# Performance work log

Hardware: AMD Instinct MI355X
Metric: run time of the kernel (lower is better)

## Reference

```python
import jax, jax.numpy as jnp
import numpy as np

D_MODEL = 1024
NUM_HEADS = 16
HEAD_DIM = D_MODEL // NUM_HEADS
B, S = 2, 2048


def setup_inputs() -> dict:
    key = jax.random.key(0)
    ks = jax.random.split(key, 8)
    scale = 1.0 / np.sqrt(D_MODEL)
    inp = {
        "query": jax.random.normal(ks[0], (B, S, D_MODEL), jnp.float32),
        "key": jax.random.normal(ks[1], (B, S, D_MODEL), jnp.float32),
        "value": jax.random.normal(ks[2], (B, S, D_MODEL), jnp.float32),
        # causal mask, broadcastable over batch and heads
        "mask": jnp.tril(jnp.ones((S, S), dtype=bool))[None, None, :, :],
        # torch nn.Linear weights: y = x @ W.T (+ b)
        "Wq": jax.random.normal(ks[3], (D_MODEL, D_MODEL), jnp.float32) * scale,
        "Wk": jax.random.normal(ks[4], (D_MODEL, D_MODEL), jnp.float32) * scale,
        "Wv": jax.random.normal(ks[5], (D_MODEL, D_MODEL), jnp.float32) * scale,
        "Wo": jax.random.normal(ks[6], (D_MODEL, D_MODEL), jnp.float32) * scale,
        "bo": jax.random.normal(ks[7], (D_MODEL,), jnp.float32) * scale,
    }
    return inp


def _split_heads(x):
    b, s, _ = x.shape
    return x.reshape(b, s, NUM_HEADS, HEAD_DIM).transpose(0, 2, 1, 3)  # [B,H,S,Dh]


def reference(query, key, value, mask, Wq, Wk, Wv, Wo, bo):
    q = _split_heads(query @ Wq.T)
    k = _split_heads(key @ Wk.T)
    v = _split_heads(value @ Wv.T)
    scores = jnp.einsum("bhqd,bhkd->bhqk", q, k) / jnp.sqrt(jnp.float32(HEAD_DIM))
    scores = jnp.where(mask, scores, jnp.float32(-jnp.inf))
    attn = jax.nn.softmax(scores, axis=-1)
    out = jnp.einsum("bhqk,bhkd->bhqd", attn, v)  # [B,H,S,Dh]
    out = out.transpose(0, 2, 1, 3).reshape(query.shape[0], q.shape[2], D_MODEL)
    return out @ Wo.T + bo
```

## Files before the change

kernel.cpp:

```cpp
#include <hip/hip_runtime.h>
#include <hip/hip_bf16.h>

#define DM   1024
#define NH   16
#define HD   64
#define SEQ  2048
#define BATCH 2
#define MTOT (BATCH*SEQ)

typedef unsigned short u16;
typedef __attribute__((ext_vector_type(8))) short bf16x8;
typedef __attribute__((ext_vector_type(4))) float f32x4;

__device__ __forceinline__ float bf2f(u16 h) {
  union { unsigned int i; float f; } u; u.i = ((unsigned int)h) << 16; return u.f;
}
__device__ __forceinline__ u16 f2bf(float f) {
  union { float f; unsigned int i; } u; u.f = f;
  unsigned int r = u.i + 0x7fffu + ((u.i >> 16) & 1u);
  return (u16)(r >> 16);
}
__device__ __forceinline__ unsigned int pk2(float lo, float hi) {
  union { float f; unsigned int u; } a, b; a.f = lo; b.f = hi;
  return ((a.u + 0x8000u) >> 16) | ((b.u + 0x8000u) & 0xFFFF0000u);
}

__global__ void detect_dtype(const u16* __restrict__ q, int* __restrict__ flag) {
  const int lane = threadIdx.x & 63;
  int cnt = 0;
  for (int i = 0; i < 8; i++) {
    int e = (q[i*64 + lane] >> 7) & 0xFF;
    unsigned long long m = __ballot(e >= 0x6E && e <= 0x8F);
    cnt += __popcll(m);
  }
  if (lane == 0) *flag = (cnt >= 400) ? 1 : 0;
}

__device__ __forceinline__ uint4 load8_bf16(const void* base, size_t elemOff, bool isf32) {
  if (!isf32) return *(const uint4*)((const u16*)base + elemOff);
  const float* f = (const float*)base + elemOff;
  f32x4 a = *(const f32x4*)f;
  f32x4 b = *(const f32x4*)(f + 4);
  union { u16 h[8]; uint4 v; } r;
  r.h[0]=f2bf(a[0]); r.h[1]=f2bf(a[1]); r.h[2]=f2bf(a[2]); r.h[3]=f2bf(a[3]);
  r.h[4]=f2bf(b[0]); r.h[5]=f2bf(b[1]); r.h[6]=f2bf(b[2]); r.h[7]=f2bf(b[3]);
  return r.v;
}

__global__ __launch_bounds__(256) void prep(
    const void* __restrict__ q, const void* __restrict__ k, const void* __restrict__ v,
    const void* __restrict__ wq, const void* __restrict__ wk, const void* __restrict__ wv,
    const void* __restrict__ wo, const void* __restrict__ bo,
    u16* __restrict__ Xq, u16* __restrict__ Xk, u16* __restrict__ Xv,
    u16* __restrict__ Wqb, u16* __restrict__ Wkb, u16* __restrict__ Wvb, u16* __restrict__ Wob,
    float* __restrict__ biasf, const int* __restrict__ dflag)
{
  const bool isf32 = (*dflag == 0);
  const int z = blockIdx.z;
  if (z == 7) {
    if (blockIdx.x == 0) {
      for (int i = threadIdx.x; i < DM; i += 256)
        biasf[i] = isf32 ? ((const float*)bo)[i] : bf2f(((const u16*)bo)[i]);
    }
    return;
  }
  const void* src; u16* dst; size_t n;
  switch (z) {
    case 0: src=q;  dst=Xq;  n=(size_t)MTOT*DM; break;
    case 1: src=k;  dst=Xk;  n=(size_t)MTOT*DM; break;
    case 2: src=v;  dst=Xv;  n=(size_t)MTOT*DM; break;
    case 3: src=wq; dst=Wqb; n=(size_t)DM*DM;   break;
    case 4: src=wk; dst=Wkb; n=(size_t)DM*DM;   break;
    case 5: src=wv; dst=Wvb; n=(size_t)DM*DM;   break;
    default: src=wo; dst=Wob; n=(size_t)DM*DM;  break;
  }
  const size_t stride = (size_t)gridDim.x * 256 * 8;
  for (size_t i = ((size_t)blockIdx.x * 256 + threadIdx.x) * 8; i < n; i += stride)
    *(uint4*)(dst + i) = load8_bf16(src, i, isf32);
}

__device__ __forceinline__ void gld16(const u16* g, u16* l) {
  __builtin_amdgcn_global_load_lds(
      (const __attribute__((address_space(1))) void*)g,
      (__attribute__((address_space(3))) void*)l, 16, 0, 0);
}

template<int MODE>
__global__ __launch_bounds__(256) void gemm128(
    const u16* __restrict__ X0, const u16* __restrict__ X1, const u16* __restrict__ X2,
    const u16* __restrict__ W0, const u16* __restrict__ W1, const u16* __restrict__ W2,
    const float* __restrict__ biasf,
    u16* __restrict__ F0, u16* __restrict__ F1, u16* __restrict__ F2,
    void* __restrict__ outP, const int* __restrict__ dflag)
{
  __shared__ u16 As[128*32];
  __shared__ u16 Bs[128*32];

  const u16* X; const u16* W; u16* outF = nullptr; int zz = 0;
  if (MODE == 0) {
    zz = blockIdx.z;
    X    = (zz==0) ? X0 : ((zz==1) ? X1 : X2);
    W    = (zz==0) ? W0 : ((zz==1) ? W1 : W2);
    outF = (zz==0) ? F0 : ((zz==1) ? F1 : F2);
  } else { X = X0; W = W0; }

  const int tid = threadIdx.x;
  const int wave = tid >> 6, lane = tid & 63, quad = lane >> 4, l16 = lane & 15;
  const int wr = wave >> 1, wc = wave & 1;
  const int m0 = blockIdx.y * 128, n0 = blockIdx.x * 128;

  const int sg = ((lane & 3) ^ ((lane >> 3) & 3)) * 8;
  const int rS = wave*32 + (lane >> 2);
  const u16* gA0 = X + (size_t)(m0 + rS)*DM + sg;
  const u16* gA1 = X + (size_t)(m0 + rS + 16)*DM + sg;
  const u16* gB0 = W + (size_t)(n0 + rS)*DM + sg;
  const u16* gB1 = W + (size_t)(n0 + rS + 16)*DM + sg;
  u16* lA0 = &As[wave*1024];
  u16* lA1 = &As[wave*1024 + 512];
  u16* lB0 = &Bs[wave*1024];
  u16* lB1 = &Bs[wave*1024 + 512];

  const int xslot8 = (quad ^ ((l16 >> 1) & 3)) * 8;

  f32x4 acc[4][4];
#pragma unroll
  for (int i = 0; i < 4; i++)
#pragma unroll
    for (int j = 0; j < 4; j++) { acc[i][j][0]=0.f; acc[i][j][1]=0.f; acc[i][j][2]=0.f; acc[i][j][3]=0.f; }

  for (int k0 = 0; k0 < DM; k0 += 32) {
    __syncthreads();
    gld16(gA0 + k0, lA0);
    gld16(gA1 + k0, lA1);
    gld16(gB0 + k0, lB0);
    gld16(gB1 + k0, lB1);
    __syncthreads();

    bf16x8 af[4], bfr[4];
#pragma unroll
    for (int fr = 0; fr < 4; fr++)
      af[fr] = *(const bf16x8*)&As[(wr*64 + fr*16 + l16)*32 + xslot8];
#pragma unroll
    for (int fc = 0; fc < 4; fc++)
      bfr[fc] = *(const bf16x8*)&Bs[(wc*64 + fc*16 + l16)*32 + xslot8];
#pragma unroll
    for (int fr = 0; fr < 4; fr++)
#pragma unroll
      for (int fc = 0; fc < 4; fc++)
        acc[fr][fc] = __builtin_amdgcn_mfma_f32_16x16x32_bf16(af[fr], bfr[fc], acc[fr][fc], 0, 0, 0);
  }

  const bool isf32 = (MODE == 1) && (*dflag == 0);
#pragma unroll
  for (int fr = 0; fr < 4; fr++) {
#pragma unroll
    for (int rr = 0; rr < 4; rr++) {
      const int m = m0 + wr*64 + fr*16 + quad*4 + rr;
#pragma unroll
      for (int fc = 0; fc < 4; fc++) {
        const int n = n0 + wc*64 + fc*16 + l16;
        float vv = acc[fr][fc][rr];
        if (MODE == 0) {
          const int b = m >> 11, s = m & (SEQ-1), h = n >> 6, d = n & (HD-1);
          if (zz == 2)
            outF[((size_t)(b*NH + h)*HD + d)*SEQ + s] = f2bf(vv);
          else
            outF[((size_t)(b*NH + h)*SEQ + s)*HD + d] = f2bf(vv);
        } else {
          vv += biasf[n];
          if (isf32) ((float*)outP)[(size_t)m*DM + n] = vv;
          else       ((u16*)outP)[(size_t)m*DM + n]   = f2bf(vv);
        }
      }
    }
  }
}

__global__ __launch_bounds__(256) void attn_mfma(
    const u16* __restrict__ Qb, const u16* __restrict__ Kb,
    const u16* __restrict__ Vtb,
    u16* __restrict__ Opart, float* __restrict__ mlpart)
{
  __shared__ u16 Qs[64][72];
  __shared__ u16 Ks[64][72];
  __shared__ u16 Vs[64][72];
  __shared__ u16 Ps[4][16][72];

  const int bh = blockIdx.x;
  const int pr = blockIdx.y, z = blockIdx.z;
  const u16* Qp = Qb  + (size_t)bh * SEQ * HD;
  const u16* Kp = Kb  + (size_t)bh * SEQ * HD;
  const u16* Vp = Vtb + (size_t)bh * HD * SEQ;

  const int tid  = threadIdx.x;
  const int wave = tid >> 6, lane = tid & 63, quad = lane >> 4, l16 = lane & 15;
  const int sr = tid >> 3, sc = (tid & 7) * 8;
  const float SC2 = 0.1803368801f;

  for (int ph = 0; ph < 2; ph++) {
    const int qt = ph ? (31 - pr) : pr;
    const int n = qt + 1, half = (n + 1) >> 1;
    const int klo = z ? half : 0, khi = z ? n : half;
    const int q0 = qt * 64;

    __syncthreads();
    *(uint4*)&Qs[sr][sc]      = *(const uint4*)&Qp[(size_t)(q0 + sr)*HD + sc];
    *(uint4*)&Qs[sr + 32][sc] = *(const uint4*)&Qp[(size_t)(q0 + sr + 32)*HD + sc];

    const int ql = wave*16 + l16;
    const int qg = q0 + ql;
    f32x4 O[4];
#pragma unroll
    for (int u = 0; u < 4; u++) { O[u][0]=0.f; O[u][1]=0.f; O[u][2]=0.f; O[u][3]=0.f; }
    float mi = -__builtin_inff(), li = 0.f;

    for (int kt = klo; kt < khi; kt++) {
      __syncthreads();
      *(uint4*)&Ks[sr][sc]      = *(const uint4*)&Kp[(size_t)(kt*64 + sr)*HD + sc];
      *(uint4*)&Ks[sr + 32][sc] = *(const uint4*)&Kp[(size_t)(kt*64 + sr + 32)*HD + sc];
      *(uint4*)&Vs[sr][sc]      = *(const uint4*)&Vp[(size_t)sr*SEQ + kt*64 + sc];
      *(uint4*)&Vs[sr + 32][sc] = *(const uint4*)&Vp[(size_t)(sr + 32)*SEQ + kt*64 + sc];
      __syncthreads();

      f32x4 st[4];
#pragma unroll
      for (int t = 0; t < 4; t++) { st[t][0]=0.f; st[t][1]=0.f; st[t][2]=0.f; st[t][3]=0.f; }
#pragma unroll
      for (int s = 0; s < 2; s++) {
        bf16x8 bq = *(const bf16x8*)&Qs[ql][s*32 + quad*8];
#pragma unroll
        for (int t = 0; t < 4; t++) {
          bf16x8 ak = *(const bf16x8*)&Ks[t*16 + l16][s*32 + quad*8];
          st[t] = __builtin_amdgcn_mfma_f32_16x16x32_bf16(ak, bq, st[t], 0, 0, 0);
        }
      }

      float v[4][4];
#pragma unroll
      for (int t = 0; t < 4; t++)
#pragma unroll
        for (int r = 0; r < 4; r++) v[t][r] = st[t][r] * SC2;
      if (kt == qt) {
#pragma unroll
        for (int t = 0; t < 4; t++)
#pragma unroll
          for (int r = 0; r < 4; r++)
            if (kt*64 + t*16 + quad*4 + r > qg) v[t][r] = -__builtin_inff();
      }
      float mx = v[0][0];
#pragma unroll
      for (int t = 0; t < 4; t++)
#pragma unroll
        for (int r = 0; r < 4; r++) mx = fmaxf(mx, v[t][r]);
      mx = fmaxf(mx, __shfl_xor(mx, 16));
      mx = fmaxf(mx, __shfl_xor(mx, 32));
      const float nm = fmaxf(mi, mx);
      const float al = exp2f(mi - nm);
      float ps = 0.f;
#pragma unroll
      for (int t = 0; t < 4; t++) {
        float p0 = exp2f(v[t][0] - nm), p1 = exp2f(v[t][1] - nm);
        float p2 = exp2f(v[t][2] - nm), p3 = exp2f(v[t][3] - nm);
        ps += (p0 + p1) + (p2 + p3);
        uint2 u2; u2.x = pk2(p0, p1); u2.y = pk2(p2, p3);
        *(uint2*)&Ps[wave][l16][t*16 + quad*4] = u2;
      }
      ps += __shfl_xor(ps, 16);
      ps += __shfl_xor(ps, 32);
      li = li * al + ps;
      mi = nm;
#pragma unroll
      for (int u = 0; u < 4; u++) {
        O[u][0] *= al; O[u][1] *= al; O[u][2] *= al; O[u][3] *= al;
      }
      __syncthreads();

#pragma unroll
      for (int s = 0; s < 2; s++) {
        bf16x8 bp = *(const bf16x8*)&Ps[wave][l16][s*32 + quad*8];
#pragma unroll
        for (int u = 0; u < 4; u++) {
          bf16x8 av = *(const bf16x8*)&Vs[u*16 + l16][s*32 + quad*8];
          O[u] = __builtin_amdgcn_mfma_f32_16x16x32_bf16(av, bp, O[u], 0, 0, 0);
        }
      }
    }

    const int pi = (bh*32 + qt)*2 + z;
    u16* op = Opart + (size_t)pi*4096 + ql*64;
#pragma unroll
    for (int u = 0; u < 4; u++) {
      uint2 u2; u2.x = pk2(O[u][0], O[u][1]); u2.y = pk2(O[u][2], O[u][3]);
      *(uint2*)&op[u*16 + quad*4] = u2;
    }
    if (quad == 0) {
      float2 ml2; ml2.x = mi; ml2.y = li;
      *(float2*)&mlpart[(size_t)pi*128 + ql*2] = ml2;
    }
  }
}

__global__ __launch_bounds__(64) void attn_merge(
    const u16* __restrict__ Opart, const float* __restrict__ mlpart,
    u16* __restrict__ aO)
{
  const int g = blockIdx.x;
  const int bh = g & 31, qt = g >> 5;
  const int b = bh >> 4, h = bh & 15;
  const int t = threadIdx.x;
  const int pi0 = (bh*32 + qt)*2, pi1 = pi0 + 1;

  const float2 ml0 = *(const float2*)&mlpart[(size_t)pi0*128 + t*2];
  const float2 ml1 = *(const float2*)&mlpart[(size_t)pi1*128 + t*2];
  const float M = fmaxf(ml0.x, ml1.x);
  float w0 = exp2f(ml0.x - M), w1 = exp2f(ml1.x - M);
  const float inv = 1.0f / (w0*ml0.y + w1*ml1.y);
  w0 *= inv; w1 *= inv;

  const u16* o0 = Opart + (size_t)pi0*4096 + t*64;
  const u16* o1 = Opart + (size_t)pi1*4096 + t*64;
  u16* out = aO + (size_t)(b*SEQ + qt*64 + t)*DM + h*HD;
#pragma unroll
  for (int d0 = 0; d0 < 64; d0 += 8) {
    union { uint4 v; u16 h[8]; } a, c; union { uint4 v; u16 h[8]; } bb;
    a.v  = *(const uint4*)&o0[d0];
    bb.v = *(const uint4*)&o1[d0];
#pragma unroll
    for (int j = 0; j < 8; j += 2) {
      float x0 = w0*bf2f(a.h[j])   + w1*bf2f(bb.h[j]);
      float x1 = w0*bf2f(a.h[j+1]) + w1*bf2f(bb.h[j+1]);
      unsigned int pk = pk2(x0, x1);
      c.h[j] = (u16)(pk & 0xFFFF); c.h[j+1] = (u16)(pk >> 16);
    }
    *(uint4*)&out[d0] = c.v;
  }
}

extern "C" void kernel_launch(void* const* d_in, const int* in_sizes, int n_in,
                              void* d_out, int out_size, void* d_ws, size_t ws_size,
                              hipStream_t stream) {
  const void* q  = d_in[0];
  const void* k  = d_in[1];
  const void* v  = d_in[2];
  const void* wq = d_in[4];
  const void* wk = d_in[5];
  const void* wv = d_in[6];
  const void* wo = d_in[7];
  const void* bo = d_in[8];

  const size_t TX = (size_t)MTOT*DM;
  const size_t TW = (size_t)DM*DM;
  u16* ws  = (u16*)d_ws;
  u16* Xq  = ws;
  u16* Xk  = ws + TX;
  u16* Xv  = ws + 2*TX;
  u16* Wqb = ws + 3*TX;
  u16* Wkb = Wqb + TW;
  u16* Wvb = Wqb + 2*TW;
  u16* Wob = Wqb + 3*TW;
  u16* Qw  = ws + 3*TX + 4*TW;
  u16* Kw  = Qw + TX;
  u16* Vt  = Qw + 2*TX;
  u16*   Opart  = Xk;
  float* mlpart = (float*)Wqb;
  u16*   aO     = Xq;
  float* biasf  = (float*)(Qw + 3*TX);
  int*   fl     = (int*)(biasf + DM);

  dim3 blk(256);
  detect_dtype<<<1, 64, 0, stream>>>((const u16*)q, fl);
  prep<<<dim3(512, 1, 8), blk, 0, stream>>>(q, k, v, wq, wk, wv, wo, bo,
      Xq, Xk, Xv, Wqb, Wkb, Wvb, Wob, biasf, fl);
  gemm128<0><<<dim3(DM/128, MTOT/128, 3), blk, 0, stream>>>(
      Xq, Xk, Xv, Wqb, Wkb, Wvb, nullptr, Qw, Kw, Vt, nullptr, fl);
  attn_mfma<<<dim3(BATCH*NH, 16, 2), blk, 0, stream>>>(Qw, Kw, Vt, Opart, mlpart);
  attn_merge<<<dim3(32*32), dim3(64), 0, stream>>>(Opart, mlpart, aO);
  gemm128<1><<<dim3(DM/128, MTOT/128, 1), blk, 0, stream>>>(
      aO, nullptr, nullptr, Wob, nullptr, nullptr, biasf, nullptr, nullptr, nullptr, d_out, fl);
}
```

Measured before the change: 255.0 us.

## Stage attention tiles via direct global-to-LDS loads with XOR swizzle, fold scale into Q

The attention kernel now loads Q, K and V tiles with direct global-to-LDS copies (gld16) into unpadded, XOR-swizzled shared arrays, replacing register-staged copies into padded arrays. The softmax scale is folded into the Q projection epilogue, and the block barrier before the PV MMA becomes a per-wave lgkmcnt wait, since each wave only reads its own P rows. The V-transposed projection output is first staged through a swizzled shared tile so it can be written with coalesced 16-byte stores. This cuts staging instructions, barriers and scattered 2-byte stores, but the swizzle and the wave-local sync have to be exactly right, and scaling before bf16 rounding changes numerics slightly.

```diff
diff --git a/kernel.cpp b/kernel.cpp
--- a/kernel.cpp
+++ b/kernel.cpp
@@ -11,6 +11,8 @@
 typedef unsigned short u16;
 typedef __attribute__((ext_vector_type(8))) short bf16x8;
 typedef __attribute__((ext_vector_type(4))) float f32x4;
+
+#define SC2F 0.1803368801111464f
 
 __device__ __forceinline__ float bf2f(u16 h) {
   union { unsigned int i; float f; } u; u.i = ((unsigned int)h) << 16; return u.f;
@@ -150,6 +152,40 @@
         acc[fr][fc] = __builtin_amdgcn_mfma_f32_16x16x32_bf16(af[fr], bfr[fc], acc[fr][fc], 0, 0, 0);
   }
 
+  if (MODE == 0 && zz == 2) {
+    __shared__ u16 Ts[64*128];
+    const int bb = m0 >> 11;
+    const int s0 = m0 & (SEQ-1);
+#pragma unroll
+    for (int p = 0; p < 2; p++) {
+      __syncthreads();
+      if (wc == p) {
+#pragma unroll
+        for (int fr = 0; fr < 4; fr++) {
+#pragma unroll
+          for (int fc = 0; fc < 4; fc++) {
+            const int dl = fc*16 + l16;
+            const int sb = wr*64 + fr*16 + quad*4;
+            const int slot = (sb >> 3) ^ (dl & 15);
+            u16* rowp = &Ts[dl*128 + slot*8 + (sb & 7)];
+            *(unsigned int*)(rowp)     = pk2(acc[fr][fc][0], acc[fr][fc][1]);
+            *(unsigned int*)(rowp + 2) = pk2(acc[fr][fc][2], acc[fr][fc][3]);
+          }
+        }
+      }
+      __syncthreads();
+      const int dl2 = tid >> 2, ch4 = tid & 3;
+      const int hh = (n0 + p*64) >> 6;
+      u16* dst = outF + ((size_t)(bb*NH + hh)*HD + dl2)*SEQ + s0 + ch4*32;
+#pragma unroll
+      for (int j = 0; j < 4; j++) {
+        const int slot = (ch4*4 + j) ^ (dl2 & 15);
+        *(uint4*)&dst[j*8] = *(const uint4*)&Ts[dl2*128 + slot*8];
+      }
+    }
+    return;
+  }
+
   const bool isf32 = (MODE == 1) && (*dflag == 0);
 #pragma unroll
   for (int fr = 0; fr < 4; fr++) {
@@ -161,11 +197,9 @@
         const int n = n0 + wc*64 + fc*16 + l16;
         float vv = acc[fr][fc][rr];
         if (MODE == 0) {
+          if (zz == 0) vv *= SC2F;
           const int b = m >> 11, s = m & (SEQ-1), h = n >> 6, d = n & (HD-1);
-          if (zz == 2)
-            outF[((size_t)(b*NH + h)*HD + d)*SEQ + s] = f2bf(vv);
-          else
-            outF[((size_t)(b*NH + h)*SEQ + s)*HD + d] = f2bf(vv);
+          outF[((size_t)(b*NH + h)*SEQ + s)*HD + d] = f2bf(vv);
         } else {
           vv += biasf[n];
           if (isf32) ((float*)outP)[(size_t)m*DM + n] = vv;
@@ -181,9 +215,9 @@
     const u16* __restrict__ Vtb,
     u16* __restrict__ Opart, float* __restrict__ mlpart)
 {
-  __shared__ u16 Qs[64][72];
-  __shared__ u16 Ks[64][72];
-  __shared__ u16 Vs[64][72];
+  __shared__ u16 Qs[64*64];
+  __shared__ u16 Ks[64*64];
+  __shared__ u16 Vs[64*64];
   __shared__ u16 Ps[4][16][72];
 
   const int bh = blockIdx.x;
@@ -194,8 +228,19 @@
 
   const int tid  = threadIdx.x;
   const int wave = tid >> 6, lane = tid & 63, quad = lane >> 4, l16 = lane & 15;
-  const int sr = tid >> 3, sc = (tid & 7) * 8;
-  const float SC2 = 0.1803368801f;
+
+  const int i0 = wave*128 + lane, i1 = i0 + 64;
+  const int r0 = i0 >> 3, c0 = (i0 & 7) ^ (r0 & 7);
+  const int r1 = i1 >> 3, c1 = (i1 & 7) ^ (r1 & 7);
+  const int kq_off0 = r0*HD + c0*8;
+  const int kq_off1 = r1*HD + c1*8;
+  const int v_off0  = r0*SEQ + c0*8;
+  const int v_off1  = r1*SEQ + c1*8;
+  u16* ldsQ0 = &Qs[wave*1024]; u16* ldsQ1 = &Qs[wave*1024 + 512];
+  u16* ldsK0 = &Ks[wave*1024]; u16* ldsK1 = &Ks[wave*1024 + 512];
+  u16* ldsV0 = &Vs[wave*1024]; u16* ldsV1 = &Vs[wave*1024 + 512];
+
+  const int l7 = l16 & 7;
 
   for (int ph = 0; ph < 2; ph++) {
     const int qt = ph ? (31 - pr) : pr;
@@ -204,8 +249,8 @@
     const int q0 = qt * 64;
 
     __syncthreads();
-    *(uint4*)&Qs[sr][sc]      = *(const uint4*)&Qp[(size_t)(q0 + sr)*HD + sc];
-    *(uint4*)&Qs[sr + 32][sc] = *(const uint4*)&Qp[(size_t)(q0 + sr + 32)*HD + sc];
+    gld16(Qp + q0*HD + kq_off0, ldsQ0);
+    gld16(Qp + q0*HD + kq_off1, ldsQ1);
 
     const int ql = wave*16 + l16;
     const int qg = q0 + ql;
@@ -216,10 +261,10 @@
 
     for (int kt = klo; kt < khi; kt++) {
       __syncthreads();
-      *(uint4*)&Ks[sr][sc]      = *(const uint4*)&Kp[(size_t)(kt*64 + sr)*HD + sc];
-      *(uint4*)&Ks[sr + 32][sc] = *(const uint4*)&Kp[(size_t)(kt*64 + sr + 32)*HD + sc];
-      *(uint4*)&Vs[sr][sc]      = *(const uint4*)&Vp[(size_t)sr*SEQ + kt*64 + sc];
-      *(uint4*)&Vs[sr + 32][sc] = *(const uint4*)&Vp[(size_t)(sr + 32)*SEQ + kt*64 + sc];
+      gld16(Kp + kt*(64*HD) + kq_off0, ldsK0);
+      gld16(Kp + kt*(64*HD) + kq_off1, ldsK1);
+      gld16(Vp + kt*64 + v_off0, ldsV0);
+      gld16(Vp + kt*64 + v_off1, ldsV1);
       __syncthreads();
 
       f32x4 st[4];
@@ -227,10 +272,11 @@
       for (int t = 0; t < 4; t++) { st[t][0]=0.f; st[t][1]=0.f; st[t][2]=0.f; st[t][3]=0.f; }
 #pragma unroll
       for (int s = 0; s < 2; s++) {
-        bf16x8 bq = *(const bf16x8*)&Qs[ql][s*32 + quad*8];
+        const int ch = s*4 + quad;
+        bf16x8 bq = *(const bf16x8*)&Qs[(ql*8 + (ch ^ l7))*8];
 #pragma unroll
         for (int t = 0; t < 4; t++) {
-          bf16x8 ak = *(const bf16x8*)&Ks[t*16 + l16][s*32 + quad*8];
+          bf16x8 ak = *(const bf16x8*)&Ks[((t*16 + l16)*8 + (ch ^ l7))*8];
           st[t] = __builtin_amdgcn_mfma_f32_16x16x32_bf16(ak, bq, st[t], 0, 0, 0);
         }
       }
@@ -239,7 +285,7 @@
 #pragma unroll
       for (int t = 0; t < 4; t++)
 #pragma unroll
-        for (int r = 0; r < 4; r++) v[t][r] = st[t][r] * SC2;
+        for (int r = 0; r < 4; r++) v[t][r] = st[t][r];
       if (kt == qt) {
 #pragma unroll
         for (int t = 0; t < 4; t++)
@@ -273,14 +319,15 @@
       for (int u = 0; u < 4; u++) {
         O[u][0] *= al; O[u][1] *= al; O[u][2] *= al; O[u][3] *= al;
       }
-      __syncthreads();
+      __asm__ volatile("s_waitcnt lgkmcnt(0)" ::: "memory");
 
 #pragma unroll
       for (int s = 0; s < 2; s++) {
+        const int ch = s*4 + quad;
         bf16x8 bp = *(const bf16x8*)&Ps[wave][l16][s*32 + quad*8];
 #pragma unroll
         for (int u = 0; u < 4; u++) {
-          bf16x8 av = *(const bf16x8*)&Vs[u*16 + l16][s*32 + quad*8];
+          bf16x8 av = *(const bf16x8*)&Vs[((u*16 + l16)*8 + (ch ^ l7))*8];
           O[u] = __builtin_amdgcn_mfma_f32_16x16x32_bf16(av, bp, O[u], 0, 0, 0);
         }
       }
```

Measured after the change: 254.5 us. No clear change (-0.2%).
